# Performance work log

Hardware: AMD Instinct MI355X
Metric: run time of the kernel (lower is better)

The kernel has to match this reference:

```python
import jax, jax.numpy as jnp
import numpy as np

B, C2, H, W = 4, 1024, 64, 64  # features have 2*input_dim channels
CH = C2 // 2                   # 512 = input_dim
HID = CH // 4                  # 128 = hidden_channels


def setup_inputs() -> dict:
    key = jax.random.key(0)
    ks = jax.random.split(key, 6)
    left = jax.random.normal(ks[0], (B, C2, H, W), dtype=jnp.float32)
    right = jax.random.normal(ks[1], (B, C2, H, W), dtype=jnp.float32)
    # 1x1 conv params (weight [out,in], bias [out]) for query/reference projections
    Wq = jax.random.normal(ks[2], (HID, CH), dtype=jnp.float32) * 0.02
    bq = jax.random.normal(ks[3], (HID,), dtype=jnp.float32) * 0.02
    Wk = jax.random.normal(ks[4], (HID, CH), dtype=jnp.float32) * 0.02
    bk = jax.random.normal(ks[5], (HID,), dtype=jnp.float32) * 0.02
    return {"left_features": left, "right_features": right, "Wq": Wq, "bq": bq, "Wk": Wk, "bk": bk}


def _co_attention(qf, rf, Wq, bq, Wk, bk):
    # 1x1 convs == per-pixel channel matmuls
    Q = jnp.einsum('bchw,oc->bohw', qf, Wq) + bq[None, :, None, None]   # [B,HID,H,W]
    K = jnp.einsum('bchw,oc->bohw', rf, Wk) + bk[None, :, None, None]   # [B,HID,H,W]
    b, c, h, w = Q.shape
    Kf = K.reshape(b, c, h * w)                                          # [B,HID,P]
    V = rf.reshape(rf.shape[0], rf.shape[1], h * w)                      # [B,CH,P]
    # attention_map: einsum('bcij,bckl->bijkl') then flatten (kl) == contract channels
    attn = jnp.einsum('bcij,bcp->bijp', Q, Kf)                           # [B,H,W,P]
    attn = jax.nn.softmax(attn, axis=3)
    return jnp.einsum('bijp,bcp->bcij', attn, V)                         # [B,CH,H,W]


def _homo(qf, rf):
    weights = jax.nn.softmax(qf - rf, axis=1)  # softmax over channels
    return rf * weights


def _get_both_differences(q, r, Wq, bq, Wk, bk):
    c = q.shape[1] // 2
    q_orig, q_trans = q[:, :c], q[:, c:]
    r_orig = r[:, :c]
    cross = _co_attention(q_orig, r_orig, Wq, bq, Wk, bk)
    reduce = _homo(q_orig, q_trans)
    return jnp.concatenate([q_orig, cross + reduce], axis=1)


def reference(left_features, right_features, Wq, bq, Wk, bk):
    left_out = _get_both_differences(left_features, right_features, Wq, bq, Wk, bk)
    right_out = _get_both_differences(right_features, left_features, Wq, bq, Wk, bk)
    return (left_out, right_out)
```

## Files before the change

### kernel.cpp

```cpp
#include <hip/hip_runtime.h>
#include <hip/hip_bf16.h>

#define NB 4
#define LOG2E 1.4426950408889634f

typedef unsigned short u16;
typedef __attribute__((ext_vector_type(8))) short bf16x8;
typedef __attribute__((ext_vector_type(4))) float f32x4;

static __device__ __forceinline__ float bf2f(u16 u) {
    union { float f; unsigned v; } x; x.v = ((unsigned)u) << 16; return x.f;
}
static __device__ __forceinline__ u16 f2bf(float f) {
    unsigned v = __builtin_bit_cast(unsigned, f);
    return (u16)((v + 0x7FFFu + ((v >> 16) & 1u)) >> 16);
}
static __device__ __forceinline__ void gload_lds16(const u16* g, u16* l) {
    __builtin_amdgcn_global_load_lds(
        (const __attribute__((address_space(1))) unsigned*)(const void*)g,
        (__attribute__((address_space(3))) unsigned*)(void*)l, 16, 0, 0);
}

__global__ void k_wcvt(const float* __restrict__ Wq, const float* __restrict__ Wk,
                       u16* __restrict__ Wbq, u16* __restrict__ Wbk) {
    int i = blockIdx.x * 1024 + threadIdx.x;
    Wbq[i] = f2bf(Wq[i]);
    Wbk[i] = f2bf(Wk[i]);
}

__global__ __launch_bounds__(256) void k_cvtf(
        const float* __restrict__ L, const float* __restrict__ R,
        u16* __restrict__ Lb, u16* __restrict__ Rb,
        u16* __restrict__ web, float* __restrict__ sumsH, float* __restrict__ out) {
    __shared__ float pred[4][1024];
    int idx = blockIdx.x;
    int sb = idx & 7, pseg = (idx >> 3) & 3, cpart = idx >> 5;
    int side = sb & 1, b = sb >> 1;
    int osb = side * 4 + b;
    const float* src = (side ? R : L) + (size_t)b * 1024 * 4096;
    u16* lbbase = (side ? Rb : Lb) + (size_t)b * 512 * 4096;
    int tid = threadIdx.x, wv = tid >> 6, lane = tid & 63;
    int p0 = pseg * 1024;
    int cA = cpart * 8 + wv * 2;
#pragma unroll
    for (int s = 0; s < 4; s++) {
        int p = p0 + s * 256 + lane * 4;
        float4 sm = {0.f, 0.f, 0.f, 0.f};
#pragma unroll
        for (int cc = 0; cc < 2; cc++) {
            int c = cA + cc;
            float4 a = *reinterpret_cast<const float4*>(src + (size_t)c * 4096 + p);
            float4 t = *reinterpret_cast<const float4*>(src + (size_t)(512 + c) * 4096 + p);
            ushort4 ub;
            ub.x = f2bf(a.x); ub.y = f2bf(a.y); ub.z = f2bf(a.z); ub.w = f2bf(a.w);
            *reinterpret_cast<ushort4*>(lbbase + (size_t)c * 4096 + p) = ub;
            *reinterpret_cast<float4*>(out + ((size_t)osb * 1024 + c) * 4096 + p) = a;
            float4 e;
            e.x = exp2f((a.x - t.x) * LOG2E);
            e.y = exp2f((a.y - t.y) * LOG2E);
            e.z = exp2f((a.z - t.z) * LOG2E);
            e.w = exp2f((a.w - t.w) * LOG2E);
            sm.x += e.x; sm.y += e.y; sm.z += e.z; sm.w += e.w;
            ushort4 wb_;
            wb_.x = f2bf(t.x * e.x); wb_.y = f2bf(t.y * e.y);
            wb_.z = f2bf(t.z * e.z); wb_.w = f2bf(t.w * e.w);
            *reinterpret_cast<ushort4*>(web + ((size_t)osb * 512 + c) * 4096 + p) = wb_;
        }
        *reinterpret_cast<float4*>(&pred[wv][s * 256 + lane * 4]) = sm;
    }
    __syncthreads();
    {
        float4 t0 = *reinterpret_cast<const float4*>(&pred[0][tid * 4]);
        float4 t1 = *reinterpret_cast<const float4*>(&pred[1][tid * 4]);
        float4 t2 = *reinterpret_cast<const float4*>(&pred[2][tid * 4]);
        float4 t3 = *reinterpret_cast<const float4*>(&pred[3][tid * 4]);
        float4 tot;
        tot.x = (t0.x + t1.x) + (t2.x + t3.x);
        tot.y = (t0.y + t1.y) + (t2.y + t3.y);
        tot.z = (t0.z + t1.z) + (t2.z + t3.z);
        tot.w = (t0.w + t1.w) + (t2.w + t3.w);
        *reinterpret_cast<float4*>(
            sumsH + ((size_t)cpart * 8 + osb) * 4096 + p0 + tid * 4) = tot;
    }
}

__global__ __launch_bounds__(256) void k_hsum(const float* __restrict__ sumsH,
                                              float* __restrict__ hinv) {
    int i = blockIdx.x * 256 + threadIdx.x;
    float4 tot = {0.f, 0.f, 0.f, 0.f};
    for (int cp = 0; cp < 64; cp++) {
        float4 v = *reinterpret_cast<const float4*>(sumsH + (size_t)cp * 8 * 4096 + (size_t)i * 4);
        tot.x += v.x; tot.y += v.y; tot.z += v.z; tot.w += v.w;
    }
    float4 r = {1.0f / tot.x, 1.0f / tot.y, 1.0f / tot.z, 1.0f / tot.w};
    *reinterpret_cast<float4*>(hinv + (size_t)i * 4) = r;
}

__global__ void k_cvt(const float* __restrict__ L, const float* __restrict__ R,
                      u16* __restrict__ Lb, u16* __restrict__ Rb, float* __restrict__ out) {
    int i = blockIdx.x * 256 + threadIdx.x;
    int pq = i & 1023;
    int c = (i >> 10) & 511;
    int b = (i >> 19) & 3;
    int side = i >> 21;
    const float* src = (side ? R : L) + ((long)(b * 1024 + c) << 12) + (pq << 2);
    float4 v = *reinterpret_cast<const float4*>(src);
    ushort4 u;
    u.x = f2bf(v.x); u.y = f2bf(v.y); u.z = f2bf(v.z); u.w = f2bf(v.w);
    *reinterpret_cast<ushort4*>((side ? Rb : Lb) + ((long)(b * 512 + c) << 12) + (pq << 2)) = u;
    *reinterpret_cast<float4*>(out + ((long)(side * 4 + b) * 1024 + c) * 4096 + (pq << 2)) = v;
}

__global__ __launch_bounds__(256) void k_proj(
        const u16* __restrict__ Lb, const u16* __restrict__ Rb,
        const u16* __restrict__ Wbq, const u16* __restrict__ Wbk,
        const float* __restrict__ bq, const float* __restrict__ bk,
        u16* __restrict__ QL, u16* __restrict__ KL,
        u16* __restrict__ QR, u16* __restrict__ KR) {
    __shared__ u16 XT[2][64 * 40];
    int pj = blockIdx.x & 15, pt = blockIdx.x >> 4;
    int ty = pj >> 2, b = pj & 3;
    const u16* src; const u16* Wb; const float* bias; u16* dst;
    if (ty == 0)      { src = Lb; Wb = Wbq; bias = bq; dst = QL; }
    else if (ty == 1) { src = Rb; Wb = Wbk; bias = bk; dst = KL; }
    else if (ty == 2) { src = Rb; Wb = Wbq; bias = bq; dst = QR; }
    else              { src = Lb; Wb = Wbk; bias = bk; dst = KR; }
    const u16* X = src + (long)b * 512 * 4096 + pt * 64;
    int tid = threadIdx.x;
    int wv = __builtin_amdgcn_readfirstlane(tid >> 6);
    int lane = tid & 63, g = lane >> 4, li = lane & 15;

    f32x4 acc[8];
#pragma unroll
    for (int ob = 0; ob < 8; ob++)
#pragma unroll
        for (int r = 0; r < 4; r++) acc[ob][r] = bias[ob * 16 + g * 4 + r];

    int c_r = tid >> 3, j = tid & 7;
    bf16x8 gx = *reinterpret_cast<const bf16x8*>(X + (long)c_r * 4096 + j * 8);
#pragma unroll
    for (int k = 0; k < 8; k++) XT[0][(j * 8 + k) * 40 + c_r] = (u16)gx[k];
    __syncthreads();

    for (int cc = 0; cc < 16; cc++) {
        int buf = cc & 1;
        bf16x8 gn;
        if (cc < 15)
            gn = *reinterpret_cast<const bf16x8*>(X + (long)(cc * 32 + 32 + c_r) * 4096 + j * 8);
        bf16x8 xb = *reinterpret_cast<const bf16x8*>(&XT[buf][(wv * 16 + li) * 40 + g * 8]);
#pragma unroll
        for (int ob = 0; ob < 8; ob++) {
            bf16x8 aw = *reinterpret_cast<const bf16x8*>(Wb + (long)(ob * 16 + li) * 512 + cc * 32 + g * 8);
            acc[ob] = __builtin_amdgcn_mfma_f32_16x16x32_bf16(aw, xb, acc[ob], 0, 0, 0);
        }
        if (cc < 15) {
#pragma unroll
            for (int k = 0; k < 8; k++) XT[buf ^ 1][(j * 8 + k) * 40 + c_r] = (u16)gn[k];
        }
        __syncthreads();
    }
    u16* d = dst + ((long)b * 4096 + pt * 64 + wv * 16 + li) * 128;
#pragma unroll
    for (int ob = 0; ob < 8; ob++) {
        uint2 w;
        w.x = (unsigned)f2bf(acc[ob][0]) | ((unsigned)f2bf(acc[ob][1]) << 16);
        w.y = (unsigned)f2bf(acc[ob][2]) | ((unsigned)f2bf(acc[ob][3]) << 16);
        *reinterpret_cast<uint2*>(d + ob * 16 + g * 4) = w;
    }
}

__global__ __launch_bounds__(512, 2) void k_qk(
        const u16* __restrict__ QL, const u16* __restrict__ KL,
        const u16* __restrict__ QR, const u16* __restrict__ KR,
        u16* __restrict__ P, float* __restrict__ sums,
        int bd0, int bdMask, int bdShift) {
    __shared__ u16 Kl[3][8192];
    __shared__ u16 Ps[4096];
    __shared__ float sred[4][2][16];
    int bdl, qtile, ph0;
    if (bdMask == 3) {
        int xcd = (int)blockIdx.x & 7;
        bdl = xcd >> 1; ph0 = xcd & 1; qtile = (int)blockIdx.x >> 3;
    } else {
        bdl = (int)blockIdx.x & bdMask;
        int rest = (int)blockIdx.x >> bdShift;
        qtile = rest & 63; ph0 = rest >> 6;
    }
    int bd = bd0 + bdl, dir = bd & 1, b = bd >> 1;
    const u16* Qt = (dir ? QR : QL) + (size_t)b * 4096 * 128;
    const u16* Kt = (dir ? KR : KL) + (size_t)b * 4096 * 128;
    u16* Pbd = P + ((size_t)bdl << 24);
    int q0 = qtile * 64;
    int tid = threadIdx.x;
    int wv = __builtin_amdgcn_readfirstlane(tid >> 6);
    int lane = tid & 63, g = lane >> 4, li = lane & 15;
    int qt = wv >> 1, phw = wv & 1;

#define STAGE_K(BUF, PT)                                                                   \
    {                                                                                      \
        _Pragma("unroll") for (int r0 = 0; r0 < 2; r0++) {                                 \
            int o = r0 * 8192 + tid * 16;                                                  \
            int row = o >> 8, w = o & 255;                                                 \
            int sw = (w ^ ((row & 7) << 4)) >> 1;                                          \
            gload_lds16(Kt + (((size_t)((PT) * 64 + row)) << 7) + sw,                      \
                        &Kl[BUF][r0 * 4096 + wv * 512]);                                   \
        }                                                                                  \
    }

    bf16x8 qf[4];
#pragma unroll
    for (int hc = 0; hc < 4; hc++)
        qf[hc] = *reinterpret_cast<const bf16x8*>(
            Qt + (size_t)(q0 + qt * 16 + li) * 128 + hc * 32 + g * 8);
    float psum = 0.f;
    STAGE_K(0, ph0 * 32)
    STAGE_K(1, ph0 * 32 + 1)

    int cur = 0;
    for (int tt = 0; tt < 32; tt++) {
        int pt = ph0 * 32 + tt;
        if (tt == 0)       asm volatile("s_waitcnt vmcnt(2) lgkmcnt(0)\n\ts_barrier" ::: "memory");
        else if (tt == 1)  asm volatile("s_waitcnt vmcnt(3) lgkmcnt(0)\n\ts_barrier" ::: "memory");
        else if (tt == 31) asm volatile("s_waitcnt vmcnt(2) lgkmcnt(0)\n\ts_barrier" ::: "memory");
        else               asm volatile("s_waitcnt vmcnt(4) lgkmcnt(0)\n\ts_barrier" ::: "memory");
        if (tt < 30) {
            int stg = cur + 2; if (stg >= 3) stg -= 3;
            STAGE_K(stg, pt + 2)
        }
        f32x4 sv[2];
        sv[0] = (f32x4){0.f, 0.f, 0.f, 0.f};
        sv[1] = (f32x4){0.f, 0.f, 0.f, 0.f};
        __builtin_amdgcn_s_setprio(1);
#pragma unroll
        for (int ps = 0; ps < 2; ps++) {
            int row = phw * 32 + ps * 16 + li;
            unsigned rb = (unsigned)row * 256;
            unsigned sz = (unsigned)((row & 7) << 4);
#pragma unroll
            for (int hc = 0; hc < 4; hc++) {
                bf16x8 kf = *reinterpret_cast<const bf16x8*>(
                    (char*)Kl[cur] + rb + (((unsigned)(hc * 64 + g * 16)) ^ sz));
                sv[ps] = __builtin_amdgcn_mfma_f32_16x16x32_bf16(kf, qf[hc], sv[ps], 0, 0, 0);
            }
        }
        __builtin_amdgcn_s_setprio(0);
        int qrow = qt * 16 + li;
        unsigned qsz = (unsigned)((qrow & 7) << 4);
#pragma unroll
        for (int ps = 0; ps < 2; ps++) {
            float e0 = exp2f(sv[ps][0] * LOG2E);
            float e1 = exp2f(sv[ps][1] * LOG2E);
            float e2 = exp2f(sv[ps][2] * LOG2E);
            float e3 = exp2f(sv[ps][3] * LOG2E);
            psum += (e0 + e1) + (e2 + e3);
            uint2 pk;
            pk.x = (unsigned)f2bf(e0) | ((unsigned)f2bf(e1) << 16);
            pk.y = (unsigned)f2bf(e2) | ((unsigned)f2bf(e3) << 16);
            unsigned off = (unsigned)qrow * 128 +
                           (((unsigned)(phw * 64 + ps * 32 + g * 8)) ^ qsz);
            *reinterpret_cast<uint2*>((char*)Ps + off) = pk;
        }
        asm volatile("s_waitcnt lgkmcnt(0)\n\ts_barrier" ::: "memory");
        {
            uint4 d = *reinterpret_cast<const uint4*>((char*)Ps + tid * 16);
            *reinterpret_cast<uint4*>(
                Pbd + ((size_t)(qtile * 64 + pt) << 12) + tid * 8) = d;
        }
        cur = (cur + 1 == 3) ? 0 : cur + 1;
    }
    psum += __shfl_xor(psum, 16);
    psum += __shfl_xor(psum, 32);
    if (lane < 16) sred[qt][phw][li] = psum;
    __syncthreads();
    if (phw == 0 && lane < 16) {
        float s = sred[qt][0][li] + sred[qt][1][li];
        sums[((size_t)ph0 * 8 + bd) * 4096 + q0 + qt * 16 + li] = s;
    }
#undef STAGE_K
}

template<int FUSEH>
__global__ __launch_bounds__(256, 2) void k_pv(
        const u16* __restrict__ Lb, const u16* __restrict__ Rb,
        const u16* __restrict__ P, const float* __restrict__ sums,
        const u16* __restrict__ web, const float* __restrict__ hinvArr,
        float* __restrict__ out, int bd0, int bdMask, int bdShift) {
    __shared__ u16 Tl[2][2][8192];
    int bdl, idx;
    if (bdMask == 3) {
        int xcd = (int)blockIdx.x & 7;
        bdl = xcd >> 1;
        idx = (((int)blockIdx.x >> 3) << 1) | (xcd & 1);
    } else {
        bdl = (int)blockIdx.x & bdMask;
        idx = (int)blockIdx.x >> bdShift;
    }
    int mtile = idx & 3;
    int ntile = idx >> 2;
    int bd = bd0 + bdl, dir = bd & 1, b = bd >> 1;
    int osb = dir * 4 + b;
    const u16* V = (dir ? Lb : Rb) + (size_t)b * 512 * 4096;
    const u16* Pbd = P + ((size_t)bdl << 24);
    int q0 = ntile * 128, c0 = mtile * 128, qt0 = ntile * 2;
    int tid = threadIdx.x;
    int wv = __builtin_amdgcn_readfirstlane(tid >> 6);
    int lane = tid & 63, g = lane >> 4, li = lane & 15;
    int wr = wv >> 1, wc = wv & 1;

#define STAGE_PV(BUF, T)                                                                   \
    {                                                                                      \
        _Pragma("unroll") for (int r0 = 0; r0 < 4; r0++) {                                 \
            int o = r0 * 4096 + tid * 16;                                                  \
            int row = o >> 7, w = o & 127;                                                 \
            int sw = (w ^ ((row & 7) << 4)) >> 1;                                          \
            gload_lds16(V + (((size_t)(c0 + row)) << 12) + (T) * 64 + sw,                  \
                        &Tl[BUF][0][r0 * 2048 + wv * 512]);                                \
            gload_lds16(Pbd + (((size_t)((qt0 + (r0 >> 1)) * 64 + (T))) << 12) +           \
                            (r0 & 1) * 2048 + tid * 8,                                     \
                        &Tl[BUF][1][r0 * 2048 + wv * 512]);                                \
        }                                                                                  \
    }

    f32x4 acc[4][4];
#pragma unroll
    for (int i = 0; i < 4; i++)
#pragma unroll
        for (int j = 0; j < 4; j++) acc[i][j] = (f32x4){0.f, 0.f, 0.f, 0.f};

    STAGE_PV(0, 0)

    for (int t = 0; t < 64; t++) {
        asm volatile("s_waitcnt vmcnt(0) lgkmcnt(0)\n\ts_barrier" ::: "memory");
        if (t < 63) STAGE_PV((t + 1) & 1, t + 1)
        int buf = t & 1;
        bf16x8 af[4][2], bf[4][2];
#pragma unroll
        for (int mi = 0; mi < 4; mi++) {
            int row = wr * 64 + mi * 16 + li;
            unsigned rb = (unsigned)row * 128, sz = (unsigned)((row & 7) << 4);
#pragma unroll
            for (int kk = 0; kk < 2; kk++)
                af[mi][kk] = *reinterpret_cast<const bf16x8*>(
                    (char*)Tl[buf][0] + rb + (((unsigned)(kk * 64 + g * 16)) ^ sz));
        }
#pragma unroll
        for (int ni = 0; ni < 4; ni++) {
            int row = wc * 64 + ni * 16 + li;
            unsigned rb = (unsigned)row * 128, sz = (unsigned)((row & 7) << 4);
#pragma unroll
            for (int kk = 0; kk < 2; kk++)
                bf[ni][kk] = *reinterpret_cast<const bf16x8*>(
                    (char*)Tl[buf][1] + rb + (((unsigned)(kk * 64 + g * 16)) ^ sz));
        }
        __builtin_amdgcn_s_setprio(1);
#pragma unroll
        for (int kk = 0; kk < 2; kk++)
#pragma unroll
            for (int mi = 0; mi < 4; mi++)
#pragma unroll
                for (int ni = 0; ni < 4; ni++)
                    acc[mi][ni] = __builtin_amdgcn_mfma_f32_16x16x32_bf16(
                        af[mi][kk], bf[ni][kk], acc[mi][ni], 0, 0, 0);
        __builtin_amdgcn_s_setprio(0);
    }

    float* obase = out + ((size_t)osb * 1024 + 512) * 4096;
    const u16* wb = web + (size_t)osb * 512 * 4096;
#pragma unroll
    for (int ni = 0; ni < 4; ni++) {
        int q = q0 + wc * 64 + ni * 16 + li;
        float s0 = sums[(size_t)bd * 4096 + q];
        float s1 = sums[((size_t)8 + bd) * 4096 + q];
        float linv = 1.0f / (s0 + s1);
        float hinv = 0.f;
        if (FUSEH) hinv = hinvArr[(size_t)osb * 4096 + q];
#pragma unroll
        for (int mi = 0; mi < 4; mi++) {
            int c = c0 + wr * 64 + mi * 16 + g * 4;
#pragma unroll
            for (int r = 0; r < 4; r++) {
                float v = acc[mi][ni][r] * linv;
                if (FUSEH) v += bf2f(wb[(size_t)(c + r) * 4096 + q]) * hinv;
                obase[(size_t)(c + r) * 4096 + q] = v;
            }
        }
    }
#undef STAGE_PV
}

__global__ __launch_bounds__(256) void k_homo(const float* __restrict__ L,
                                              const float* __restrict__ R,
                                              float* __restrict__ out) {
    __shared__ float4 red[16][16];
    int sb = blockIdx.x & 7, pblk = blockIdx.x >> 3;
    int side = sb & 1, b = sb >> 1;
    const float* src = (side ? R : L) + (long)b * 1024 * 4096;
    float* o = out + (long)(side * 4 + b) * 1024 * 4096;
    int p4 = threadIdx.x & 15, cg = threadIdx.x >> 4;
    int p = pblk * 64 + p4 * 4;
    const float* qo = src + p;
    const float* qt = src + (long)512 * 4096 + p;
    float4 sm = {0.f, 0.f, 0.f, 0.f};
    for (int c = cg * 32; c < cg * 32 + 32; c++) {
        float4 a = *reinterpret_cast<const float4*>(qo + (long)c * 4096);
        float4 t = *reinterpret_cast<const float4*>(qt + (long)c * 4096);
        sm.x += exp2f((a.x - t.x) * LOG2E);
        sm.y += exp2f((a.y - t.y) * LOG2E);
        sm.z += exp2f((a.z - t.z) * LOG2E);
        sm.w += exp2f((a.w - t.w) * LOG2E);
    }
    red[cg][p4] = sm;
    __syncthreads();
    float4 tot = {0.f, 0.f, 0.f, 0.f};
#pragma unroll
    for (int gR = 0; gR < 16; gR++) {
        float4 v = red[gR][p4];
        tot.x += v.x; tot.y += v.y; tot.z += v.z; tot.w += v.w;
    }
    float4 rinv = {1.0f / tot.x, 1.0f / tot.y, 1.0f / tot.z, 1.0f / tot.w};
    for (int c = cg * 32; c < cg * 32 + 32; c++) {
        float4 a = *reinterpret_cast<const float4*>(qo + (long)c * 4096);
        float4 t = *reinterpret_cast<const float4*>(qt + (long)c * 4096);
        float4* op = reinterpret_cast<float4*>(o + (long)(512 + c) * 4096 + p);
        float4 cur = *op;
        cur.x += t.x * exp2f((a.x - t.x) * LOG2E) * rinv.x;
        cur.y += t.y * exp2f((a.y - t.y) * LOG2E) * rinv.y;
        cur.z += t.z * exp2f((a.z - t.z) * LOG2E) * rinv.z;
        cur.w += t.w * exp2f((a.w - t.w) * LOG2E) * rinv.w;
        *op = cur;
    }
}

extern "C" void kernel_launch(void* const* d_in, const int* in_sizes, int n_in,
                              void* d_out, int out_size, void* d_ws, size_t ws_size,
                              hipStream_t stream) {
    const float* L  = (const float*)d_in[0];
    const float* R  = (const float*)d_in[1];
    const float* Wq = (const float*)d_in[2];
    const float* bq = (const float*)d_in[3];
    const float* Wk = (const float*)d_in[4];
    const float* bk = (const float*)d_in[5];
    float* out = (float*)d_out;
    char* ws = (char*)d_ws;

    size_t off = 0;
    u16* Wbq = (u16*)(ws + off); off += (size_t)128 * 512 * 2;
    u16* Wbk = (u16*)(ws + off); off += (size_t)128 * 512 * 2;
    u16* QL = (u16*)(ws + off); off += (size_t)NB * 4096 * 128 * 2;
    u16* KL = (u16*)(ws + off); off += (size_t)NB * 4096 * 128 * 2;
    u16* QR = (u16*)(ws + off); off += (size_t)NB * 4096 * 128 * 2;
    u16* KR = (u16*)(ws + off); off += (size_t)NB * 4096 * 128 * 2;
    u16* Lb = (u16*)(ws + off); off += (size_t)NB * 512 * 4096 * 2;
    u16* Rb = (u16*)(ws + off); off += (size_t)NB * 512 * 4096 * 2;
    float* sums = (float*)(ws + off); off += (size_t)2 * 8 * 4096 * 4;
    float* hinv = (float*)(ws + off); off += (size_t)8 * 4096 * 4;
    size_t off_nofuse = off;
    float* sumsH = (float*)(ws + off); off += (size_t)64 * 8 * 4096 * 4;
    u16* web = (u16*)(ws + off); off += (size_t)8 * 512 * 4096 * 2;
    off = (off + 255) & ~(size_t)255;
    size_t pchunk4 = (size_t)4 * 4096 * 4096 * 2;

    k_wcvt <<<64, 1024, 0, stream>>>(Wq, Wk, Wbq, Wbk);

    if (ws_size >= off + pchunk4) {
        u16* Pb = (u16*)(ws + off);
        k_cvtf <<<2048, 256, 0, stream>>>(L, R, Lb, Rb, web, sumsH, out);
        k_hsum <<<32,   256, 0, stream>>>(sumsH, hinv);
        k_proj <<<1024, 256, 0, stream>>>(Lb, Rb, Wbq, Wbk, bq, bk, QL, KL, QR, KR);
        for (int c = 0; c < 2; c++) {
            k_qk    <<<512, 512, 0, stream>>>(QL, KL, QR, KR, Pb, sums, c * 4, 3, 2);
            k_pv<1> <<<512, 256, 0, stream>>>(Lb, Rb, Pb, sums, web, hinv, out, c * 4, 3, 2);
        }
    } else {
        int nbd, bdShift;
        size_t poff = (off_nofuse + 255) & ~(size_t)255;
        if (ws_size >= poff + pchunk4) { nbd = 4; bdShift = 2; }
        else                           { nbd = 1; bdShift = 0; }
        int bdMask = nbd - 1, nchunk = 8 / nbd;
        u16* Pb = (u16*)(ws + poff);
        k_cvt  <<<16384, 256, 0, stream>>>(L, R, Lb, Rb, out);
        k_proj <<<1024,  256, 0, stream>>>(Lb, Rb, Wbq, Wbk, bq, bk, QL, KL, QR, KR);
        for (int c = 0; c < nchunk; c++) {
            k_qk    <<<nbd * 128, 512, 0, stream>>>(QL, KL, QR, KR, Pb, sums,
                                                    c * nbd, bdMask, bdShift);
            k_pv<0> <<<nbd * 128, 256, 0, stream>>>(Lb, Rb, Pb, sums, web, hinv, out,
                                                    c * nbd, bdMask, bdShift);
        }
        k_homo <<<512, 256, 0, stream>>>(L, R, out);
    }
}
```

Baseline: 406.6 us.

## Triple-buffer PV kernel with half-size K tiles and partial vmcnt waits

The PV GEMM kernel's LDS staging changes from a double buffer of 64-wide K tiles to a triple buffer of 32-wide K tiles. Loads are issued two stages ahead, and the wait uses vmcnt(4) so the barrier no longer drains every outstanding global load. Source pointers and swizzled LDS offsets are precomputed once outside the loop. The goal is better overlap of global-to-LDS copies with MFMA work. The cost is twice as many barriers, and the smaller tile changes LDS use and possibly bank-conflict behaviour.

```diff
diff --git a/kernel.cpp b/kernel.cpp
--- a/kernel.cpp
+++ b/kernel.cpp
@@ -285,7 +285,7 @@
         const u16* __restrict__ P, const float* __restrict__ sums,
         const u16* __restrict__ web, const float* __restrict__ hinvArr,
         float* __restrict__ out, int bd0, int bdMask, int bdShift) {
-    __shared__ u16 Tl[2][2][8192];
+    __shared__ u16 Tl[3][2][4096];
     int bdl, idx;
     if (bdMask == 3) {
         int xcd = (int)blockIdx.x & 7;
@@ -307,18 +307,40 @@
     int lane = tid & 63, g = lane >> 4, li = lane & 15;
     int wr = wv >> 1, wc = wv & 1;
 
-#define STAGE_PV(BUF, T)                                                                   \
+    const u16* vsrc[2];
+    const u16* psrc[2][2];
+#pragma unroll
+    for (int r0 = 0; r0 < 2; r0++) {
+        int o = r0 * 4096 + tid * 16;
+        int row = o >> 6, w = o & 63;
+        int qrow = row & 63;
+        int lw = w ^ ((row & 3) << 4);
+        vsrc[r0] = V + (((size_t)(c0 + row)) << 12) + (lw >> 1);
+#pragma unroll
+        for (int pc = 0; pc < 2; pc++) {
+            int gb = ((pc * 64 + lw) ^ ((qrow & 7) << 4)) >> 1;
+            psrc[r0][pc] = Pbd + (((size_t)((qt0 + (row >> 6)) * 64)) << 12) + qrow * 64 + gb;
+        }
+    }
+    unsigned aoff[4], boff[4];
+#pragma unroll
+    for (int mi = 0; mi < 4; mi++) {
+        int row = wr * 64 + mi * 16 + li;
+        aoff[mi] = (unsigned)row * 64 + (((unsigned)(g * 16)) ^ ((row & 3) << 4));
+    }
+#pragma unroll
+    for (int ni = 0; ni < 4; ni++) {
+        int row = wc * 64 + ni * 16 + li;
+        boff[ni] = (unsigned)row * 64 + (((unsigned)(g * 16)) ^ ((row & 3) << 4));
+    }
+
+#define STAGE_H(BUF, T)                                                                    \
     {                                                                                      \
-        _Pragma("unroll") for (int r0 = 0; r0 < 4; r0++) {                                 \
-            int o = r0 * 4096 + tid * 16;                                                  \
-            int row = o >> 7, w = o & 127;                                                 \
-            int sw = (w ^ ((row & 7) << 4)) >> 1;                                          \
-            gload_lds16(V + (((size_t)(c0 + row)) << 12) + (T) * 64 + sw,                  \
-                        &Tl[BUF][0][r0 * 2048 + wv * 512]);                                \
-            gload_lds16(Pbd + (((size_t)((qt0 + (r0 >> 1)) * 64 + (T))) << 12) +           \
-                            (r0 & 1) * 2048 + tid * 8,                                     \
-                        &Tl[BUF][1][r0 * 2048 + wv * 512]);                                \
-        }                                                                                  \
+        int pt_ = (T) >> 1, pc_ = (T) & 1;                                                 \
+        gload_lds16(vsrc[0] + (T) * 32, &Tl[BUF][0][wv * 512]);                            \
+        gload_lds16(vsrc[1] + (T) * 32, &Tl[BUF][0][2048 + wv * 512]);                     \
+        gload_lds16(psrc[0][pc_] + pt_ * 4096, &Tl[BUF][1][wv * 512]);                     \
+        gload_lds16(psrc[1][pc_] + pt_ * 4096, &Tl[BUF][1][2048 + wv * 512]);              \
     }
 
     f32x4 acc[4][4];
@@ -327,41 +349,33 @@
 #pragma unroll
         for (int j = 0; j < 4; j++) acc[i][j] = (f32x4){0.f, 0.f, 0.f, 0.f};
 
-    STAGE_PV(0, 0)
-
-    for (int t = 0; t < 64; t++) {
-        asm volatile("s_waitcnt vmcnt(0) lgkmcnt(0)\n\ts_barrier" ::: "memory");
-        if (t < 63) STAGE_PV((t + 1) & 1, t + 1)
-        int buf = t & 1;
-        bf16x8 af[4][2], bf[4][2];
-#pragma unroll
-        for (int mi = 0; mi < 4; mi++) {
-            int row = wr * 64 + mi * 16 + li;
-            unsigned rb = (unsigned)row * 128, sz = (unsigned)((row & 7) << 4);
-#pragma unroll
-            for (int kk = 0; kk < 2; kk++)
-                af[mi][kk] = *reinterpret_cast<const bf16x8*>(
-                    (char*)Tl[buf][0] + rb + (((unsigned)(kk * 64 + g * 16)) ^ sz));
-        }
-#pragma unroll
-        for (int ni = 0; ni < 4; ni++) {
-            int row = wc * 64 + ni * 16 + li;
-            unsigned rb = (unsigned)row * 128, sz = (unsigned)((row & 7) << 4);
-#pragma unroll
-            for (int kk = 0; kk < 2; kk++)
-                bf[ni][kk] = *reinterpret_cast<const bf16x8*>(
-                    (char*)Tl[buf][1] + rb + (((unsigned)(kk * 64 + g * 16)) ^ sz));
-        }
+    STAGE_H(0, 0)
+    STAGE_H(1, 1)
+
+    int cur = 0;
+    for (int t = 0; t < 128; t++) {
+        if (t < 127) asm volatile("s_waitcnt vmcnt(4) lgkmcnt(0)\n\ts_barrier" ::: "memory");
+        else         asm volatile("s_waitcnt vmcnt(0) lgkmcnt(0)\n\ts_barrier" ::: "memory");
+        if (t < 126) {
+            int stg = cur + 2; if (stg >= 3) stg -= 3;
+            STAGE_H(stg, t + 2)
+        }
+        bf16x8 af[4], bf[4];
+#pragma unroll
+        for (int mi = 0; mi < 4; mi++)
+            af[mi] = *reinterpret_cast<const bf16x8*>((char*)Tl[cur][0] + aoff[mi]);
+#pragma unroll
+        for (int ni = 0; ni < 4; ni++)
+            bf[ni] = *reinterpret_cast<const bf16x8*>((char*)Tl[cur][1] + boff[ni]);
         __builtin_amdgcn_s_setprio(1);
 #pragma unroll
-        for (int kk = 0; kk < 2; kk++)
-#pragma unroll
-            for (int mi = 0; mi < 4; mi++)
-#pragma unroll
-                for (int ni = 0; ni < 4; ni++)
-                    acc[mi][ni] = __builtin_amdgcn_mfma_f32_16x16x32_bf16(
-                        af[mi][kk], bf[ni][kk], acc[mi][ni], 0, 0, 0);
+        for (int mi = 0; mi < 4; mi++)
+#pragma unroll
+            for (int ni = 0; ni < 4; ni++)
+                acc[mi][ni] = __builtin_amdgcn_mfma_f32_16x16x32_bf16(
+                    af[mi], bf[ni], acc[mi][ni], 0, 0, 0);
         __builtin_amdgcn_s_setprio(0);
+        cur = (cur + 1 == 3) ? 0 : cur + 1;
     }
 
     float* obase = out + ((size_t)osb * 1024 + 512) * 4096;
@@ -385,7 +399,7 @@
             }
         }
     }
-#undef STAGE_PV
+#undef STAGE_H
 }
 
 __global__ __launch_bounds__(256) void k_homo(const float* __restrict__ L,
```

Result: slower. 424.3 us (+4.3%).

## Materialize full P for all batch-directions and add large-tile PV kernel

Applied to the files above, without the earlier changes.

When the workspace holds the full P matrix for all 8 batch-directions, QK runs as one 1024-block launch and a new k_pv8 kernel does PV with 256x256 output tiles per 512-thread block, using a 4-slot global-to-LDS pipeline. This removes the two-chunk launch loop and the smaller tiles of the old PV kernel, which raises operand reuse and reduces launch and tail overhead. In exchange it needs double the P workspace, launches only 256 PV blocks (one wave at most on the GPU), and holds a 128-register accumulator per thread, which may limit occupancy. The no-fuse fallback is simplified to one bd per chunk.

```diff
diff --git a/kernel.cpp b/kernel.cpp
--- a/kernel.cpp
+++ b/kernel.cpp
@@ -280,7 +280,134 @@
 }
 
 template<int FUSEH>
-__global__ __launch_bounds__(256, 2) void k_pv(
+__global__ __launch_bounds__(512, 2) void k_pv8(
+        const u16* __restrict__ Lb, const u16* __restrict__ Rb,
+        const u16* __restrict__ P, const float* __restrict__ sums,
+        const u16* __restrict__ web, const float* __restrict__ hinvArr,
+        float* __restrict__ out) {
+    __shared__ u16 Vl[4][8192];
+    __shared__ u16 Pl[4][8192];
+    int bd = (int)blockIdx.x & 7;
+    int idx = (int)blockIdx.x >> 3;
+    int mt = idx & 1, nt = idx >> 1;
+    int dir = bd & 1, b = bd >> 1, osb = dir * 4 + b;
+    const u16* V = (dir ? Lb : Rb) + (size_t)b * 512 * 4096;
+    const u16* Pbd = P + ((size_t)bd << 24);
+    int c0 = mt * 256, q0 = nt * 256;
+    int tid = threadIdx.x;
+    int wv = __builtin_amdgcn_readfirstlane(tid >> 6);
+    int lane = tid & 63, g = lane >> 4, li = lane & 15;
+    int wr = wv >> 2, wc = wv & 3;
+
+    const u16 *vs0, *vs1, *pb0, *pb1;
+    int pOff0a, pOff0b, pOff1a, pOff1b;
+    {
+        int o = tid * 16;
+        int row = o >> 6, w = o & 63;
+        int sw = ((row >> 1) & 3) << 4;
+        int wd = w ^ sw;
+        vs0 = V + (size_t)(c0 + row) * 4096 + (wd >> 1);
+        int q = q0 + row, qtile = q >> 6, qr = q & 63;
+        pb0 = Pbd + (size_t)(qtile * 64) * 4096 + qr * 64;
+        pOff0a = ((wd) ^ ((qr & 7) << 4)) >> 1;
+        pOff0b = ((64 + wd) ^ ((qr & 7) << 4)) >> 1;
+    }
+    {
+        int o = 8192 + tid * 16;
+        int row = o >> 6, w = o & 63;
+        int sw = ((row >> 1) & 3) << 4;
+        int wd = w ^ sw;
+        vs1 = V + (size_t)(c0 + row) * 4096 + (wd >> 1);
+        int q = q0 + row, qtile = q >> 6, qr = q & 63;
+        pb1 = Pbd + (size_t)(qtile * 64) * 4096 + qr * 64;
+        pOff1a = ((wd) ^ ((qr & 7) << 4)) >> 1;
+        pOff1b = ((64 + wd) ^ ((qr & 7) << 4)) >> 1;
+    }
+
+#define STAGE8(SLOT, T)                                                                    \
+    {                                                                                      \
+        gload_lds16(vs0 + (T) * 32, &Vl[SLOT][tid * 8]);                                   \
+        gload_lds16(vs1 + (T) * 32, &Vl[SLOT][4096 + tid * 8]);                            \
+        gload_lds16(pb0 + ((T) >> 1) * 4096 + (((T) & 1) ? pOff0b : pOff0a),               \
+                    &Pl[SLOT][tid * 8]);                                                   \
+        gload_lds16(pb1 + ((T) >> 1) * 4096 + (((T) & 1) ? pOff1b : pOff1a),               \
+                    &Pl[SLOT][4096 + tid * 8]);                                            \
+    }
+
+    unsigned aoff[8], boff[4];
+#pragma unroll
+    for (int mi = 0; mi < 8; mi++) {
+        int row = wr * 128 + mi * 16 + li;
+        aoff[mi] = (unsigned)row * 64 + (((unsigned)(g * 16)) ^ (((row >> 1) & 3) << 4));
+    }
+#pragma unroll
+    for (int ni = 0; ni < 4; ni++) {
+        int row = wc * 64 + ni * 16 + li;
+        boff[ni] = (unsigned)row * 64 + (((unsigned)(g * 16)) ^ (((row >> 1) & 3) << 4));
+    }
+
+    f32x4 acc[8][4];
+#pragma unroll
+    for (int i = 0; i < 8; i++)
+#pragma unroll
+        for (int j = 0; j < 4; j++) acc[i][j] = (f32x4){0.f, 0.f, 0.f, 0.f};
+
+    STAGE8(0, 0)
+    STAGE8(1, 1)
+    STAGE8(2, 2)
+
+    for (int t = 0; t < 128; t++) {
+        if (t < 126)       asm volatile("s_waitcnt vmcnt(8) lgkmcnt(0)\n\ts_barrier" ::: "memory");
+        else if (t == 126) asm volatile("s_waitcnt vmcnt(4) lgkmcnt(0)\n\ts_barrier" ::: "memory");
+        else               asm volatile("s_waitcnt vmcnt(0) lgkmcnt(0)\n\ts_barrier" ::: "memory");
+        if (t < 125) {
+            int slot = (t + 3) & 3;
+            STAGE8(slot, t + 3)
+        }
+        int cur = t & 3;
+        bf16x8 af[8], bf[4];
+#pragma unroll
+        for (int mi = 0; mi < 8; mi++)
+            af[mi] = *reinterpret_cast<const bf16x8*>((char*)Vl[cur] + aoff[mi]);
+#pragma unroll
+        for (int ni = 0; ni < 4; ni++)
+            bf[ni] = *reinterpret_cast<const bf16x8*>((char*)Pl[cur] + boff[ni]);
+        __builtin_amdgcn_s_setprio(1);
+#pragma unroll
+        for (int mi = 0; mi < 8; mi++)
+#pragma unroll
+            for (int ni = 0; ni < 4; ni++)
+                acc[mi][ni] = __builtin_amdgcn_mfma_f32_16x16x32_bf16(
+                    af[mi], bf[ni], acc[mi][ni], 0, 0, 0);
+        __builtin_amdgcn_s_setprio(0);
+    }
+
+    float* obase = out + ((size_t)osb * 1024 + 512) * 4096;
+    const u16* wb = web + (size_t)osb * 512 * 4096;
+#pragma unroll
+    for (int ni = 0; ni < 4; ni++) {
+        int q = q0 + wc * 64 + ni * 16 + li;
+        float s0 = sums[(size_t)bd * 4096 + q];
+        float s1 = sums[((size_t)8 + bd) * 4096 + q];
+        float linv = 1.0f / (s0 + s1);
+        float hinv = 0.f;
+        if (FUSEH) hinv = hinvArr[(size_t)osb * 4096 + q];
+#pragma unroll
+        for (int mi = 0; mi < 8; mi++) {
+            int c = c0 + wr * 128 + mi * 16 + g * 4;
+#pragma unroll
+            for (int r = 0; r < 4; r++) {
+                float v = acc[mi][ni][r] * linv;
+                if (FUSEH) v += bf2f(wb[(size_t)(c + r) * 4096 + q]) * hinv;
+                obase[(size_t)(c + r) * 4096 + q] = v;
+            }
+        }
+    }
+#undef STAGE8
+}
+
+template<int FUSEH>
+__global__ __launch_bounds__(256, 2) void k_pvC(
         const u16* __restrict__ Lb, const u16* __restrict__ Rb,
         const u16* __restrict__ P, const float* __restrict__ sums,
         const u16* __restrict__ web, const float* __restrict__ hinvArr,
@@ -459,32 +586,34 @@
     u16* web = (u16*)(ws + off); off += (size_t)8 * 512 * 4096 * 2;
     off = (off + 255) & ~(size_t)255;
     size_t pchunk4 = (size_t)4 * 4096 * 4096 * 2;
+    size_t pfull   = (size_t)8 * 4096 * 4096 * 2;
 
     k_wcvt <<<64, 1024, 0, stream>>>(Wq, Wk, Wbq, Wbk);
 
-    if (ws_size >= off + pchunk4) {
+    if (ws_size >= off + pfull) {
+        u16* Pb = (u16*)(ws + off);
+        k_cvtf   <<<2048, 256, 0, stream>>>(L, R, Lb, Rb, web, sumsH, out);
+        k_hsum   <<<32,   256, 0, stream>>>(sumsH, hinv);
+        k_proj   <<<1024, 256, 0, stream>>>(Lb, Rb, Wbq, Wbk, bq, bk, QL, KL, QR, KR);
+        k_qk     <<<1024, 512, 0, stream>>>(QL, KL, QR, KR, Pb, sums, 0, 7, 3);
+        k_pv8<1> <<<256,  512, 0, stream>>>(Lb, Rb, Pb, sums, web, hinv, out);
+    } else if (ws_size >= off + pchunk4) {
         u16* Pb = (u16*)(ws + off);
         k_cvtf <<<2048, 256, 0, stream>>>(L, R, Lb, Rb, web, sumsH, out);
         k_hsum <<<32,   256, 0, stream>>>(sumsH, hinv);
         k_proj <<<1024, 256, 0, stream>>>(Lb, Rb, Wbq, Wbk, bq, bk, QL, KL, QR, KR);
         for (int c = 0; c < 2; c++) {
-            k_qk    <<<512, 512, 0, stream>>>(QL, KL, QR, KR, Pb, sums, c * 4, 3, 2);
-            k_pv<1> <<<512, 256, 0, stream>>>(Lb, Rb, Pb, sums, web, hinv, out, c * 4, 3, 2);
+            k_qk     <<<512, 512, 0, stream>>>(QL, KL, QR, KR, Pb, sums, c * 4, 3, 2);
+            k_pvC<1> <<<512, 256, 0, stream>>>(Lb, Rb, Pb, sums, web, hinv, out, c * 4, 3, 2);
         }
     } else {
-        int nbd, bdShift;
         size_t poff = (off_nofuse + 255) & ~(size_t)255;
-        if (ws_size >= poff + pchunk4) { nbd = 4; bdShift = 2; }
-        else                           { nbd = 1; bdShift = 0; }
-        int bdMask = nbd - 1, nchunk = 8 / nbd;
         u16* Pb = (u16*)(ws + poff);
         k_cvt  <<<16384, 256, 0, stream>>>(L, R, Lb, Rb, out);
         k_proj <<<1024,  256, 0, stream>>>(Lb, Rb, Wbq, Wbk, bq, bk, QL, KL, QR, KR);
-        for (int c = 0; c < nchunk; c++) {
-            k_qk    <<<nbd * 128, 512, 0, stream>>>(QL, KL, QR, KR, Pb, sums,
-                                                    c * nbd, bdMask, bdShift);
-            k_pv<0> <<<nbd * 128, 256, 0, stream>>>(Lb, Rb, Pb, sums, web, hinv, out,
-                                                    c * nbd, bdMask, bdShift);
+        for (int c = 0; c < 8; c++) {
+            k_qk     <<<128, 512, 0, stream>>>(QL, KL, QR, KR, Pb, sums, c, 0, 0);
+            k_pvC<0> <<<128, 256, 0, stream>>>(Lb, Rb, Pb, sums, web, hinv, out, c, 0, 0);
         }
         k_homo <<<512, 256, 0, stream>>>(L, R, out);
     }
```

Result: slower. 463.6 us (+14.0%).

## Split QK key range into four phases per block with double-buffered K staging

Applied to the files above, without the earlier changes.

The QK/exp kernel now splits the 4096 keys into four phases of 16 tiles instead of two phases of 32, doubling the grid. It replaces the triple-buffered K staging with a double buffer and reuses the Ps buffer for the row-sum reduction, which cuts LDS use. Launch bounds are raised to allow more resident waves. The PV kernel now sums four partial row sums instead of two. This trades a shallower prefetch pipeline and more partial-sum traffic for more parallelism and occupancy. The workspace-limited fallback path drops its 4-directions-per-chunk option and always launches one direction at a time.

```diff
diff --git a/kernel.cpp b/kernel.cpp
--- a/kernel.cpp
+++ b/kernel.cpp
@@ -169,23 +169,18 @@
     }
 }
 
-__global__ __launch_bounds__(512, 2) void k_qk(
+__global__ __launch_bounds__(512, 8) void k_qk(
         const u16* __restrict__ QL, const u16* __restrict__ KL,
         const u16* __restrict__ QR, const u16* __restrict__ KR,
         u16* __restrict__ P, float* __restrict__ sums,
-        int bd0, int bdMask, int bdShift) {
-    __shared__ u16 Kl[3][8192];
+        int bd0, int nbdLog2) {
+    __shared__ u16 Kl[2][8192];
     __shared__ u16 Ps[4096];
-    __shared__ float sred[4][2][16];
-    int bdl, qtile, ph0;
-    if (bdMask == 3) {
-        int xcd = (int)blockIdx.x & 7;
-        bdl = xcd >> 1; ph0 = xcd & 1; qtile = (int)blockIdx.x >> 3;
-    } else {
-        bdl = (int)blockIdx.x & bdMask;
-        int rest = (int)blockIdx.x >> bdShift;
-        qtile = rest & 63; ph0 = rest >> 6;
-    }
+    int blk = (int)blockIdx.x;
+    int bdl = blk & ((1 << nbdLog2) - 1);
+    int rest = blk >> nbdLog2;
+    int ph0 = rest & 3;
+    int qtile = rest >> 2;
     int bd = bd0 + bdl, dir = bd & 1, b = bd >> 1;
     const u16* Qt = (dir ? QR : QL) + (size_t)b * 4096 * 128;
     const u16* Kt = (dir ? KR : KL) + (size_t)b * 4096 * 128;
@@ -213,20 +208,14 @@
         qf[hc] = *reinterpret_cast<const bf16x8*>(
             Qt + (size_t)(q0 + qt * 16 + li) * 128 + hc * 32 + g * 8);
     float psum = 0.f;
-    STAGE_K(0, ph0 * 32)
-    STAGE_K(1, ph0 * 32 + 1)
-
-    int cur = 0;
-    for (int tt = 0; tt < 32; tt++) {
-        int pt = ph0 * 32 + tt;
-        if (tt == 0)       asm volatile("s_waitcnt vmcnt(2) lgkmcnt(0)\n\ts_barrier" ::: "memory");
-        else if (tt == 1)  asm volatile("s_waitcnt vmcnt(3) lgkmcnt(0)\n\ts_barrier" ::: "memory");
-        else if (tt == 31) asm volatile("s_waitcnt vmcnt(2) lgkmcnt(0)\n\ts_barrier" ::: "memory");
-        else               asm volatile("s_waitcnt vmcnt(4) lgkmcnt(0)\n\ts_barrier" ::: "memory");
-        if (tt < 30) {
-            int stg = cur + 2; if (stg >= 3) stg -= 3;
-            STAGE_K(stg, pt + 2)
-        }
+    STAGE_K(0, ph0 * 16)
+
+    for (int tt = 0; tt < 16; tt++) {
+        int pt = ph0 * 16 + tt;
+        if (tt == 0) asm volatile("s_waitcnt vmcnt(0) lgkmcnt(0)\n\ts_barrier" ::: "memory");
+        else         asm volatile("s_waitcnt vmcnt(1) lgkmcnt(0)\n\ts_barrier" ::: "memory");
+        if (tt < 15) STAGE_K((tt + 1) & 1, pt + 1)
+        int buf = tt & 1;
         f32x4 sv[2];
         sv[0] = (f32x4){0.f, 0.f, 0.f, 0.f};
         sv[1] = (f32x4){0.f, 0.f, 0.f, 0.f};
@@ -239,7 +228,7 @@
 #pragma unroll
             for (int hc = 0; hc < 4; hc++) {
                 bf16x8 kf = *reinterpret_cast<const bf16x8*>(
-                    (char*)Kl[cur] + rb + (((unsigned)(hc * 64 + g * 16)) ^ sz));
+                    (char*)Kl[buf] + rb + (((unsigned)(hc * 64 + g * 16)) ^ sz));
                 sv[ps] = __builtin_amdgcn_mfma_f32_16x16x32_bf16(kf, qf[hc], sv[ps], 0, 0, 0);
             }
         }
@@ -266,8 +255,9 @@
             *reinterpret_cast<uint4*>(
                 Pbd + ((size_t)(qtile * 64 + pt) << 12) + tid * 8) = d;
         }
-        cur = (cur + 1 == 3) ? 0 : cur + 1;
-    }
+    }
+    __syncthreads();
+    float (*sred)[2][16] = (float(*)[2][16])(void*)Ps;
     psum += __shfl_xor(psum, 16);
     psum += __shfl_xor(psum, 32);
     if (lane < 16) sred[qt][phw][li] = psum;
@@ -280,7 +270,7 @@
 }
 
 template<int FUSEH>
-__global__ __launch_bounds__(256, 2) void k_pv(
+__global__ __launch_bounds__(256, 2) void k_pvC(
         const u16* __restrict__ Lb, const u16* __restrict__ Rb,
         const u16* __restrict__ P, const float* __restrict__ sums,
         const u16* __restrict__ web, const float* __restrict__ hinvArr,
@@ -369,9 +359,11 @@
 #pragma unroll
     for (int ni = 0; ni < 4; ni++) {
         int q = q0 + wc * 64 + ni * 16 + li;
-        float s0 = sums[(size_t)bd * 4096 + q];
-        float s1 = sums[((size_t)8 + bd) * 4096 + q];
-        float linv = 1.0f / (s0 + s1);
+        float s = sums[(size_t)bd * 4096 + q] +
+                  sums[((size_t)8 + bd) * 4096 + q] +
+                  sums[((size_t)16 + bd) * 4096 + q] +
+                  sums[((size_t)24 + bd) * 4096 + q];
+        float linv = 1.0f / s;
         float hinv = 0.f;
         if (FUSEH) hinv = hinvArr[(size_t)osb * 4096 + q];
 #pragma unroll
@@ -452,7 +444,7 @@
     u16* KR = (u16*)(ws + off); off += (size_t)NB * 4096 * 128 * 2;
     u16* Lb = (u16*)(ws + off); off += (size_t)NB * 512 * 4096 * 2;
     u16* Rb = (u16*)(ws + off); off += (size_t)NB * 512 * 4096 * 2;
-    float* sums = (float*)(ws + off); off += (size_t)2 * 8 * 4096 * 4;
+    float* sums = (float*)(ws + off); off += (size_t)4 * 8 * 4096 * 4;
     float* hinv = (float*)(ws + off); off += (size_t)8 * 4096 * 4;
     size_t off_nofuse = off;
     float* sumsH = (float*)(ws + off); off += (size_t)64 * 8 * 4096 * 4;
@@ -468,23 +460,17 @@
         k_hsum <<<32,   256, 0, stream>>>(sumsH, hinv);
         k_proj <<<1024, 256, 0, stream>>>(Lb, Rb, Wbq, Wbk, bq, bk, QL, KL, QR, KR);
         for (int c = 0; c < 2; c++) {
-            k_qk    <<<512, 512, 0, stream>>>(QL, KL, QR, KR, Pb, sums, c * 4, 3, 2);
-            k_pv<1> <<<512, 256, 0, stream>>>(Lb, Rb, Pb, sums, web, hinv, out, c * 4, 3, 2);
+            k_qk     <<<1024, 512, 0, stream>>>(QL, KL, QR, KR, Pb, sums, c * 4, 2);
+            k_pvC<1> <<<512,  256, 0, stream>>>(Lb, Rb, Pb, sums, web, hinv, out, c * 4, 3, 2);
         }
     } else {
-        int nbd, bdShift;
         size_t poff = (off_nofuse + 255) & ~(size_t)255;
-        if (ws_size >= poff + pchunk4) { nbd = 4; bdShift = 2; }
-        else                           { nbd = 1; bdShift = 0; }
-        int bdMask = nbd - 1, nchunk = 8 / nbd;
         u16* Pb = (u16*)(ws + poff);
         k_cvt  <<<16384, 256, 0, stream>>>(L, R, Lb, Rb, out);
         k_proj <<<1024,  256, 0, stream>>>(Lb, Rb, Wbq, Wbk, bq, bk, QL, KL, QR, KR);
-        for (int c = 0; c < nchunk; c++) {
-            k_qk    <<<nbd * 128, 512, 0, stream>>>(QL, KL, QR, KR, Pb, sums,
-                                                    c * nbd, bdMask, bdShift);
-            k_pv<0> <<<nbd * 128, 256, 0, stream>>>(Lb, Rb, Pb, sums, web, hinv, out,
-                                                    c * nbd, bdMask, bdShift);
+        for (int c = 0; c < 8; c++) {
+            k_qk     <<<256, 512, 0, stream>>>(QL, KL, QR, KR, Pb, sums, c, 0);
+            k_pvC<0> <<<128, 256, 0, stream>>>(Lb, Rb, Pb, sums, web, hinv, out, c, 0, 0);
         }
         k_homo <<<512, 256, 0, stream>>>(L, R, out);
     }
```

After: 381.6 us (median of 2 runs). 1.07x faster.
